# Kernel optimization log

Hardware: AMD Instinct MI355X
Metric: run time of the kernel (lower is better)

The kernel has to match this reference:

```python
import jax, jax.numpy as jnp
import numpy as np

B, S, D, F = 8, 2048, 256, 8

def setup_inputs() -> dict:
    key = jax.random.key(0)
    ks = jax.random.split(key, 7)
    hidden_states = jax.random.normal(ks[0], (B, S, D), dtype=jnp.float32)
    # flat indices into zero-prepended [1 + B*S, D] token table; 0 = padding row
    select_idx = jax.random.randint(ks[1], (B, S, F), 0, B * S + 1, dtype=jnp.int32)
    word_mask = jax.random.randint(ks[2], (B, S), 0, 2, dtype=jnp.int32)
    W1 = jax.random.normal(ks[3], (D, D), dtype=jnp.float32) * (1.0 / np.sqrt(D))
    b1 = jax.random.normal(ks[4], (D,), dtype=jnp.float32) * 0.02
    w2 = jax.random.normal(ks[5], (D,), dtype=jnp.float32) * (1.0 / np.sqrt(D))
    b2 = jax.random.normal(ks[6], (1,), dtype=jnp.float32) * 0.02
    return {"hidden_states": hidden_states, "select_idx": select_idx,
            "word_mask": word_mask, "W1": W1, "b1": b1, "w2": w2, "b2": b2}

def reference(hidden_states, select_idx, word_mask, W1, b1, w2, b2):
    b, s, d = hidden_states.shape
    h = jnp.tanh(hidden_states.reshape(-1, d) @ W1.T + b1)          # [B*S, D]
    h = jnp.concatenate([jnp.zeros((1, d), h.dtype), h], axis=0)    # zero padding row at index 0
    g = h[select_idx.reshape(-1)]                                    # gather: [B*S*F, D]
    g = g.reshape(b * s, -1, d).max(axis=1)                          # AdaptiveMaxPool1d(1) over word occurrences
    scores = (g @ w2 + b2[0]).reshape(b, s)                          # w2 linear -> [B, S]
    neg = -10000.0 * (1.0 - word_mask.astype(jnp.float32))
    return scores.astype(jnp.float32) + neg
```

## Files before the change

### kernel.cpp

```cpp
#include <hip/hip_runtime.h>
#include <hip/hip_bf16.h>
#include <math.h>

#define BB 8
#define SS 2048
#define DD 256
#define FF 8
#define NTOK (BB*SS)

typedef __bf16 bf16x8 __attribute__((ext_vector_type(8)));
typedef float  f32x4  __attribute__((ext_vector_type(4)));
typedef float  f32x2  __attribute__((ext_vector_type(2)));

#define BM 128
#define BN 64
#define BK 64
#define NSTEP (DD/BK)
#define XS 72

__device__ __forceinline__ float fast_tanh(float x) {
    float e = __expf(2.0f * x);
    return 1.0f - 2.0f * __builtin_amdgcn_rcpf(e + 1.0f);
}

__device__ __forceinline__ unsigned pack2_bf16(float a, float b) {
    return (__float_as_uint(a) >> 16) | (__float_as_uint(b) & 0xFFFF0000u);
}

__device__ __forceinline__ unsigned char f32_to_fp8(float v) {
    return (unsigned char)(__builtin_amdgcn_cvt_pk_fp8_f32(v, v, 0, false) & 0xFF);
}

__global__ __launch_bounds__(512, 4) void gemm_tanh_kernel(
    const float* __restrict__ x, const float* __restrict__ W1,
    const float* __restrict__ b1, unsigned char* __restrict__ table)
{
    __shared__ __align__(16) unsigned short xs[2][BM * XS];
    __shared__ __align__(16) unsigned short wsb[2][BN * XS];

    const int tid  = threadIdx.x;
    const int bx   = blockIdx.x;
    const int tokgrp = bx & 127;
    const int nblk   = bx >> 7;
    const int tok0 = tokgrp * BM;
    const int n0   = nblk * BN;

    if (bx == 0 && tid < 64) ((unsigned int*)table)[tid] = 0u;

    const int wave = tid >> 6, lane = tid & 63;
    const int wm = wave >> 1;
    const int wn = wave & 1;
    const int lr = lane & 15;
    const int kg = lane >> 4;

    f32x4 xr[4], wr[2];

    auto load_chunk = [&](int k0) {
        #pragma unroll
        for (int rep = 0; rep < 4; ++rep) {
            int slot = rep * 512 + tid;
            int row = slot >> 4, kc = slot & 15;
            xr[rep] = *(const f32x4*)&x[(size_t)(tok0 + row) * DD + k0 + kc * 4];
        }
        #pragma unroll
        for (int rep = 0; rep < 2; ++rep) {
            int slot = rep * 512 + tid;
            int row = slot >> 4, kc = slot & 15;
            wr[rep] = *(const f32x4*)&W1[(size_t)(n0 + row) * DD + k0 + kc * 4];
        }
    };
    auto store_lds = [&](int buf) {
        #pragma unroll
        for (int rep = 0; rep < 4; ++rep) {
            int slot = rep * 512 + tid;
            int row = slot >> 4, kc = slot & 15;
            uint2 p;
            p.x = pack2_bf16(xr[rep].x, xr[rep].y);
            p.y = pack2_bf16(xr[rep].z, xr[rep].w);
            *(uint2*)&xs[buf][row * XS + kc * 4] = p;
        }
        #pragma unroll
        for (int rep = 0; rep < 2; ++rep) {
            int slot = rep * 512 + tid;
            int row = slot >> 4, kc = slot & 15;
            uint2 p;
            p.x = pack2_bf16(wr[rep].x, wr[rep].y);
            p.y = pack2_bf16(wr[rep].z, wr[rep].w);
            *(uint2*)&wsb[buf][row * XS + kc * 4] = p;
        }
    };

    f32x4 acc[2][2];
    #pragma unroll
    for (int mf = 0; mf < 2; ++mf)
        #pragma unroll
        for (int nf = 0; nf < 2; ++nf)
            acc[mf][nf] = (f32x4){0.f, 0.f, 0.f, 0.f};

    load_chunk(0);
    store_lds(0);

    for (int s = 0; s < NSTEP; ++s) {
        __syncthreads();
        const int buf = s & 1;
        if (s + 1 < NSTEP) load_chunk((s + 1) * BK);

        bf16x8 af[2][2], bfr[2][2];
        #pragma unroll
        for (int c = 0; c < 2; ++c) {
            #pragma unroll
            for (int mf = 0; mf < 2; ++mf) {
                int m = wm * 32 + mf * 16 + lr;
                af[c][mf] = *(const bf16x8*)&xs[buf][m * XS + c * 32 + kg * 8];
            }
            #pragma unroll
            for (int nf = 0; nf < 2; ++nf) {
                int n = wn * 32 + nf * 16 + lr;
                bfr[c][nf] = *(const bf16x8*)&wsb[buf][n * XS + c * 32 + kg * 8];
            }
        }
        if (s + 1 < NSTEP) store_lds(buf ^ 1);

        #pragma unroll
        for (int c = 0; c < 2; ++c)
            #pragma unroll
            for (int mf = 0; mf < 2; ++mf)
                #pragma unroll
                for (int nf = 0; nf < 2; ++nf)
                    acc[mf][nf] = __builtin_amdgcn_mfma_f32_16x16x32_bf16(
                        af[c][mf], bfr[c][nf], acc[mf][nf], 0, 0, 0);
    }

    float bj[2];
    #pragma unroll
    for (int nf = 0; nf < 2; ++nf) bj[nf] = b1[n0 + wn * 32 + nf * 16 + lr];

    __syncthreads();
    unsigned char* sc = (unsigned char*)&xs[0][0];
    #pragma unroll
    for (int mf = 0; mf < 2; ++mf) {
        #pragma unroll
        for (int r = 0; r < 4; ++r) {
            int m = wm * 32 + mf * 16 + kg * 4 + r;
            #pragma unroll
            for (int nf = 0; nf < 2; ++nf) {
                float v = fast_tanh(acc[mf][nf][r] + bj[nf]);
                sc[m * 80 + wn * 32 + nf * 16 + lr] = f32_to_fp8(v);
            }
        }
    }
    __syncthreads();
    {
        int row = tid >> 2;
        int off = (tid & 3) * 16;
        uint4 v = *(const uint4*)&sc[row * 80 + off];
        *(uint4*)&table[(size_t)(1 + tok0 + row) * DD + n0 + off] = v;
    }
}

__global__ __launch_bounds__(256) void gather_score_kernel(
    const unsigned char* __restrict__ table,
    const int* __restrict__ select_idx,
    const int* __restrict__ word_mask,
    const float* __restrict__ w2,
    const float* __restrict__ b2,
    float* __restrict__ out)
{
    const int tid  = threadIdx.x;
    const int lane = tid & 63;
    const int wv   = tid >> 6;
    const int i    = blockIdx.x * 4 + wv;
    const int half = lane >> 5;
    const int c    = lane & 31;
    const int d0   = c * 8;

    const int4* sp = (const int4*)(select_idx + (size_t)i * FF);
    int4 q0 = sp[0], q1 = sp[1];
    int rows[4];
    rows[0] = half ? q0.y : q0.x;
    rows[1] = half ? q0.w : q0.z;
    rows[2] = half ? q1.y : q1.x;
    rows[3] = half ? q1.w : q1.z;

    float m[8];
    #pragma unroll
    for (int j = 0; j < 8; ++j) m[j] = -INFINITY;

    #pragma unroll
    for (int it = 0; it < 4; ++it) {
        uint2 u = *(const uint2*)(table + (size_t)rows[it] * DD + d0);
        f32x2 a0 = __builtin_amdgcn_cvt_pk_f32_fp8(u.x, false);
        f32x2 a1 = __builtin_amdgcn_cvt_pk_f32_fp8(u.x, true);
        f32x2 a2 = __builtin_amdgcn_cvt_pk_f32_fp8(u.y, false);
        f32x2 a3 = __builtin_amdgcn_cvt_pk_f32_fp8(u.y, true);
        m[0] = fmaxf(m[0], a0.x); m[1] = fmaxf(m[1], a0.y);
        m[2] = fmaxf(m[2], a1.x); m[3] = fmaxf(m[3], a1.y);
        m[4] = fmaxf(m[4], a2.x); m[5] = fmaxf(m[5], a2.y);
        m[6] = fmaxf(m[6], a3.x); m[7] = fmaxf(m[7], a3.y);
    }

    #pragma unroll
    for (int j = 0; j < 8; ++j) m[j] = fmaxf(m[j], __shfl_xor(m[j], 32));

    f32x4 wa = *(const f32x4*)&w2[d0];
    f32x4 wb = *(const f32x4*)&w2[d0 + 4];
    float p = m[0] * wa.x + m[1] * wa.y + m[2] * wa.z + m[3] * wa.w
            + m[4] * wb.x + m[5] * wb.y + m[6] * wb.z + m[7] * wb.w;

    #pragma unroll
    for (int off = 16; off; off >>= 1) p += __shfl_xor(p, off);

    if (lane == 0) {
        float neg = word_mask[i] ? 0.f : -10000.f;
        out[i] = p + b2[0] + neg;
    }
}

extern "C" void kernel_launch(void* const* d_in, const int* in_sizes, int n_in,
                              void* d_out, int out_size, void* d_ws, size_t ws_size,
                              hipStream_t stream) {
    const float* hs    = (const float*)d_in[0];
    const int*   sidx  = (const int*)  d_in[1];
    const int*   wmask = (const int*)  d_in[2];
    const float* W1    = (const float*)d_in[3];
    const float* b1    = (const float*)d_in[4];
    const float* w2    = (const float*)d_in[5];
    const float* b2    = (const float*)d_in[6];
    float* out = (float*)d_out;

    unsigned char* table = (unsigned char*)d_ws;

    gemm_tanh_kernel<<<(NTOK / BM) * (DD / BN), 512, 0, stream>>>(hs, W1, b1, table);
    gather_score_kernel<<<NTOK / 4, 256, 0, stream>>>(table, sidx, wmask, w2, b2, out);
}
```

Before: 85.75 us.

## Keep W1 fragments in registers and halve GEMM token tile

Each wave now loads its W1 slice once at kernel start, converts it to bf16 and keeps it as MFMA B-fragments in registers. This removes the W1 staging through LDS and its per-step LDS reads. The token tile drops from 128 to 64 rows with 256-thread blocks, so the grid doubles. The cost is about 64 extra VGPRs per lane, which may reduce occupancy, and W1 is read from global memory by more blocks.

```diff
diff --git a/kernel.cpp b/kernel.cpp
--- a/kernel.cpp
+++ b/kernel.cpp
@@ -12,7 +12,7 @@
 typedef float  f32x4  __attribute__((ext_vector_type(4)));
 typedef float  f32x2  __attribute__((ext_vector_type(2)));
 
-#define BM 128
+#define BM 64
 #define BN 64
 #define BK 64
 #define NSTEP (DD/BK)
@@ -31,17 +31,16 @@
     return (unsigned char)(__builtin_amdgcn_cvt_pk_fp8_f32(v, v, 0, false) & 0xFF);
 }
 
-__global__ __launch_bounds__(512, 4) void gemm_tanh_kernel(
+__global__ __launch_bounds__(256, 4) void gemm_tanh_kernel(
     const float* __restrict__ x, const float* __restrict__ W1,
     const float* __restrict__ b1, unsigned char* __restrict__ table)
 {
     __shared__ __align__(16) unsigned short xs[2][BM * XS];
-    __shared__ __align__(16) unsigned short wsb[2][BN * XS];
 
     const int tid  = threadIdx.x;
     const int bx   = blockIdx.x;
-    const int tokgrp = bx & 127;
-    const int nblk   = bx >> 7;
+    const int tokgrp = bx & 255;
+    const int nblk   = bx >> 8;
     const int tok0 = tokgrp * BM;
     const int n0   = nblk * BN;
 
@@ -53,41 +52,44 @@
     const int lr = lane & 15;
     const int kg = lane >> 4;
 
-    f32x4 xr[4], wr[2];
+    bf16x8 bfrg[8][2];
+    #pragma unroll
+    for (int kc = 0; kc < 8; ++kc) {
+        #pragma unroll
+        for (int nf = 0; nf < 2; ++nf) {
+            int n = n0 + wn * 32 + nf * 16 + lr;
+            const float* p = &W1[(size_t)n * DD + kc * 32 + kg * 8];
+            f32x4 lo = *(const f32x4*)p;
+            f32x4 hi = *(const f32x4*)(p + 4);
+            uint4 pk;
+            pk.x = pack2_bf16(lo.x, lo.y);
+            pk.y = pack2_bf16(lo.z, lo.w);
+            pk.z = pack2_bf16(hi.x, hi.y);
+            pk.w = pack2_bf16(hi.z, hi.w);
+            bfrg[kc][nf] = __builtin_bit_cast(bf16x8, pk);
+        }
+    }
+
+    f32x4 xr[4];
 
     auto load_chunk = [&](int k0) {
         #pragma unroll
         for (int rep = 0; rep < 4; ++rep) {
-            int slot = rep * 512 + tid;
+            int slot = rep * 256 + tid;
             int row = slot >> 4, kc = slot & 15;
             xr[rep] = *(const f32x4*)&x[(size_t)(tok0 + row) * DD + k0 + kc * 4];
         }
-        #pragma unroll
-        for (int rep = 0; rep < 2; ++rep) {
-            int slot = rep * 512 + tid;
-            int row = slot >> 4, kc = slot & 15;
-            wr[rep] = *(const f32x4*)&W1[(size_t)(n0 + row) * DD + k0 + kc * 4];
-        }
     };
     auto store_lds = [&](int buf) {
         #pragma unroll
         for (int rep = 0; rep < 4; ++rep) {
-            int slot = rep * 512 + tid;
+            int slot = rep * 256 + tid;
             int row = slot >> 4, kc = slot & 15;
             uint2 p;
             p.x = pack2_bf16(xr[rep].x, xr[rep].y);
             p.y = pack2_bf16(xr[rep].z, xr[rep].w);
             *(uint2*)&xs[buf][row * XS + kc * 4] = p;
         }
-        #pragma unroll
-        for (int rep = 0; rep < 2; ++rep) {
-            int slot = rep * 512 + tid;
-            int row = slot >> 4, kc = slot & 15;
-            uint2 p;
-            p.x = pack2_bf16(wr[rep].x, wr[rep].y);
-            p.y = pack2_bf16(wr[rep].z, wr[rep].w);
-            *(uint2*)&wsb[buf][row * XS + kc * 4] = p;
-        }
     };
 
     f32x4 acc[2][2];
@@ -100,25 +102,20 @@
     load_chunk(0);
     store_lds(0);
 
+    #pragma unroll
     for (int s = 0; s < NSTEP; ++s) {
         __syncthreads();
         const int buf = s & 1;
         if (s + 1 < NSTEP) load_chunk((s + 1) * BK);
 
-        bf16x8 af[2][2], bfr[2][2];
-        #pragma unroll
-        for (int c = 0; c < 2; ++c) {
+        bf16x8 af[2][2];
+        #pragma unroll
+        for (int c = 0; c < 2; ++c)
             #pragma unroll
             for (int mf = 0; mf < 2; ++mf) {
                 int m = wm * 32 + mf * 16 + lr;
                 af[c][mf] = *(const bf16x8*)&xs[buf][m * XS + c * 32 + kg * 8];
             }
-            #pragma unroll
-            for (int nf = 0; nf < 2; ++nf) {
-                int n = wn * 32 + nf * 16 + lr;
-                bfr[c][nf] = *(const bf16x8*)&wsb[buf][n * XS + c * 32 + kg * 8];
-            }
-        }
         if (s + 1 < NSTEP) store_lds(buf ^ 1);
 
         #pragma unroll
@@ -128,7 +125,7 @@
                 #pragma unroll
                 for (int nf = 0; nf < 2; ++nf)
                     acc[mf][nf] = __builtin_amdgcn_mfma_f32_16x16x32_bf16(
-                        af[c][mf], bfr[c][nf], acc[mf][nf], 0, 0, 0);
+                        af[c][mf], bfrg[s * 2 + c][nf], acc[mf][nf], 0, 0, 0);
     }
 
     float bj[2];
@@ -230,6 +227,6 @@
 
     unsigned char* table = (unsigned char*)d_ws;
 
-    gemm_tanh_kernel<<<(NTOK / BM) * (DD / BN), 512, 0, stream>>>(hs, W1, b1, table);
+    gemm_tanh_kernel<<<(NTOK / BM) * (DD / BN), 256, 0, stream>>>(hs, W1, b1, table);
     gather_score_kernel<<<NTOK / 4, 256, 0, stream>>>(table, sidx, wmask, w2, b2, out);
 }
```

Result: slower. 101.3 us (+18.1%).
